# Performance work log

Hardware: AMD Instinct MI355X
Metric: run time of the kernel (lower is better)

The kernel has to match this reference:

```python
import jax, jax.numpy as jnp
import numpy as np

B, N, D = 4, 4096, 1024
QK = D // 8          # qk_dim_div = 8 -> 128
E = 2 * D            # expand_factor = 2 -> 2048


def setup_inputs() -> dict:
    key = jax.random.key(0)
    k1, k2, k3 = jax.random.split(key, 3)
    x = jax.random.normal(k1, (B, N, D), dtype=jnp.float32)
    # xavier-uniform-like scale for the fused expand / project weights
    expand = jax.random.normal(k2, (D, 2 * QK + 2 * E), dtype=jnp.float32) * np.sqrt(2.0 / (D + 2 * QK + 2 * E)).astype(np.float32)
    project = jax.random.normal(k3, (E, D), dtype=jnp.float32) * np.sqrt(2.0 / (E + D)).astype(np.float32)
    position_bias_mult = jnp.float32(4.0)
    return {"x": x, "expand": expand, "project": project, "position_bias_mult": position_bias_mult}


def _layer_norm(x, eps=1e-5):
    mu = jnp.mean(x, axis=-1, keepdims=True)
    var = jnp.mean(jnp.square(x - mu), axis=-1, keepdims=True)
    return (x - mu) * jax.lax.rsqrt(var + eps)


def reference(x, expand, project, position_bias_mult):
    d = x.shape[-1]
    qk, e = d // 8, 2 * d
    n = x.shape[1]

    nx = _layer_norm(x)
    h = nx @ expand                                    # [B, N, 2*qk + 2*e]
    q = h[..., :qk]
    k = h[..., qk:2 * qk]
    linear = h[..., 2 * qk:2 * qk + e]
    pre_gelu = h[..., 2 * qk + e:]

    gated = linear * jax.nn.gelu(pre_gelu, approximate=False)  # torch F.gelu = exact erf
    local = gated[..., :e - d]                          # [B, N, e-d]
    v = gated[..., e - d:]                              # [B, N, d]

    # learned sigmoid position bias under causal mask
    pos = jnp.arange(n)
    base = (pos[None, :] - pos[:, None]).astype(x.dtype)  # j - i
    causal = pos[None, :] <= pos[:, None]
    mask = jnp.where(causal, jax.nn.sigmoid(base + position_bias_mult), -jnp.inf)

    logits = jnp.einsum('bnq,bmq->bnm', q, k) / np.sqrt(qk).astype(np.float32) + mask
    scores = jax.nn.softmax(logits, axis=-1)            # [B, N, N]
    attn = jnp.einsum('bnm,bmd->bnd', scores, v)         # [B, N, d]

    return x + jnp.concatenate([local, attn], axis=-1) @ project
```

## Files before the change

### kernel.cpp

```cpp
#include <hip/hip_runtime.h>
#include <type_traits>

typedef __bf16 bf16x8 __attribute__((ext_vector_type(8)));
typedef __bf16 bf16x4v __attribute__((ext_vector_type(4)));
typedef float f32x4 __attribute__((ext_vector_type(4)));
typedef unsigned short u16x8 __attribute__((ext_vector_type(8)));
typedef unsigned short u16x4 __attribute__((ext_vector_type(4)));

#define NSEQ 4096
#define DM 1024
#define NBATCH 4

__device__ __forceinline__ unsigned short f2bf(float f) {
  unsigned u = __float_as_uint(f);
  u += 0x7FFFu + ((u >> 16) & 1u);
  return (unsigned short)(u >> 16);
}
__device__ __forceinline__ float bf2f(unsigned short h) {
  return __uint_as_float(((unsigned)h) << 16);
}
__device__ __forceinline__ float gelu_fast(float x) {
  const float y = 1.5957691216057308f * (x + 0.044715f * x * x * x);
  return x / (1.0f + __expf(-y));
}

__device__ __forceinline__ void gload_lds16(const unsigned short* src,
                                            unsigned short* dst) {
  __builtin_amdgcn_global_load_lds(
      (const __attribute__((address_space(1))) unsigned int*)src,
      (__attribute__((address_space(3))) unsigned int*)dst, 16, 0, 0);
}

#define BAR() asm volatile("s_barrier" ::: "memory")
#define VMCNT8() asm volatile("s_waitcnt vmcnt(8)" ::: "memory")

__device__ __forceinline__ int perm_col(int n) {
  if (n < 256) return n;
  int c = n - 256;
  if (c < 2048) return 256 + ((c >> 5) << 6) + (c & 31);
  c -= 2048;
  return 256 + ((c >> 5) << 6) + 32 + (c & 31);
}

__global__ __launch_bounds__(256) void ln_kernel(const float* __restrict__ x,
                                                 unsigned short* __restrict__ nx) {
  const int row = blockIdx.x;
  const int tid = threadIdx.x;
  const float4 v = reinterpret_cast<const float4*>(x + (size_t)row * DM)[tid];
  float s = v.x + v.y + v.z + v.w;
  float q = v.x * v.x + v.y * v.y + v.z * v.z + v.w * v.w;
#pragma unroll
  for (int off = 32; off > 0; off >>= 1) {
    s += __shfl_down(s, off);
    q += __shfl_down(q, off);
  }
  __shared__ float ss[4], sq[4];
  if ((tid & 63) == 0) {
    ss[tid >> 6] = s;
    sq[tid >> 6] = q;
  }
  __syncthreads();
  const float ts = ss[0] + ss[1] + ss[2] + ss[3];
  const float tq = sq[0] + sq[1] + sq[2] + sq[3];
  const float mu = ts * (1.0f / DM);
  const float var = tq * (1.0f / DM) - mu * mu;
  const float rs = rsqrtf(var + 1e-5f);
  u16x4 o;
  o[0] = f2bf((v.x - mu) * rs);
  o[1] = f2bf((v.y - mu) * rs);
  o[2] = f2bf((v.z - mu) * rs);
  o[3] = f2bf((v.w - mu) * rs);
  *reinterpret_cast<u16x4*>(nx + (size_t)row * DM + tid * 4) = o;
}

template <bool PERM>
__global__ __launch_bounds__(256) void tconv_kernel(const float* __restrict__ in,
                                                    unsigned short* __restrict__ out,
                                                    int K, int N) {
  __shared__ unsigned short tile[64][72];
  const int n0 = blockIdx.x * 64;
  const int k0 = blockIdx.y * 64;
  const int tid = threadIdx.x;
  const int lr = tid >> 4, lc = (tid & 15) * 4;
#pragma unroll
  for (int p = 0; p < 4; p++) {
    const int r = lr + p * 16;
    float4 v = *reinterpret_cast<const float4*>(in + (size_t)(k0 + r) * N + n0 + lc);
    tile[r][lc + 0] = f2bf(v.x);
    tile[r][lc + 1] = f2bf(v.y);
    tile[r][lc + 2] = f2bf(v.z);
    tile[r][lc + 3] = f2bf(v.w);
  }
  __syncthreads();
  const int nn = tid >> 2, kkg = (tid & 3) * 16;
  u16x8 o0, o1;
#pragma unroll
  for (int j = 0; j < 8; j++) {
    o0[j] = tile[kkg + j][nn];
    o1[j] = tile[kkg + 8 + j][nn];
  }
  const int orow = PERM ? perm_col(n0 + nn) : (n0 + nn);
  unsigned short* dst = out + (size_t)orow * K + k0 + kkg;
  *reinterpret_cast<u16x8*>(dst) = o0;
  *reinterpret_cast<u16x8*>(dst + 8) = o1;
}

template <int MODE>
__global__ __launch_bounds__(512, 2) void gemm256_kernel(
    const unsigned short* __restrict__ A, int lda,
    const unsigned short* __restrict__ Bt, int ldb, void* __restrict__ Cv,
    void* __restrict__ Cv2, int ldc, int K, int ntn,
    const float* __restrict__ X) {
  __shared__ unsigned short Ah[2][2][8192];
  __shared__ unsigned short Bh[2][2][8192];
  const int tid = threadIdx.x;
  const int lane = tid & 63;
  const int w = tid >> 6;
  const int lq = lane & 15;
  const int lg = lane >> 4;
  const int wm = w >> 2;
  const int wn = w & 3;
  const int bid = blockIdx.x;
  const int m0 = (bid / ntn) * 256;
  const int n0 = (bid % ntn) * 256;
  const int nk = K >> 6;

  const int g0 = w * 64 + lane;
  const int rowS = g0 >> 2;
  const int kcS = ((g0 & 3) * 8) ^ (((rowS >> 1) & 3) << 3);
  const unsigned short* Asrc = A + (size_t)(m0 + rowS) * lda + kcS;
  const unsigned short* Bsrc = Bt + (size_t)(n0 + rowS) * ldb + kcS;
  const size_t ldaj = (size_t)128 * lda;
  const size_t ldbj = (size_t)128 * ldb;
  const int dstW = w * 64 * 8;

  auto stageA = [&](int db, int kh, int kt2) {
    if (kt2 < nk) {
      const unsigned short* s = Asrc + (size_t)kt2 * 64 + kh * 32;
      unsigned short* d = &Ah[db][kh][0] + dstW;
      gload_lds16(s, d);
      gload_lds16(s + ldaj, d + 4096);
    }
  };
  auto stageB = [&](int db, int kh, int kt2) {
    if (kt2 < nk) {
      const unsigned short* s = Bsrc + (size_t)kt2 * 64 + kh * 32;
      unsigned short* d = &Bh[db][kh][0] + dstW;
      gload_lds16(s, d);
      gload_lds16(s + ldbj, d + 4096);
    }
  };

  f32x4 acc[8][4];
#pragma unroll
  for (int i = 0; i < 8; i++)
#pragma unroll
    for (int j = 0; j < 4; j++)
#pragma unroll
      for (int r = 0; r < 4; r++) acc[i][j][r] = 0.0f;

  stageA(0, 0, 0);
  stageB(0, 0, 0);
  stageA(0, 1, 0);
  stageB(0, 1, 0);
  stageA(1, 0, 1);
  stageB(1, 0, 1);
  VMCNT8();
  BAR();

  const int aBase = wm * 128;
  const int bBase = wn * 64;
  const int cSwz = (lg * 8) ^ (((lq >> 1) & 3) << 3);

#pragma unroll 1
  for (int kt = 0; kt < nk; ++kt) {
    const int buf = kt & 1;
    bf16x8 af[4], bf0[4], bf1[4];

#pragma unroll
    for (int i = 0; i < 4; i++)
      af[i] = *reinterpret_cast<const bf16x8*>(
          &Ah[buf][0][(aBase + i * 16 + lq) * 32 + cSwz]);
#pragma unroll
    for (int j = 0; j < 4; j++)
      bf0[j] = *reinterpret_cast<const bf16x8*>(
          &Bh[buf][0][(bBase + j * 16 + lq) * 32 + cSwz]);
    stageA(buf ^ 1, 1, kt + 1);
    BAR();
    __builtin_amdgcn_s_setprio(1);
#pragma unroll
    for (int i = 0; i < 4; i++)
#pragma unroll
      for (int j = 0; j < 4; j++)
        acc[i][j] =
            __builtin_amdgcn_mfma_f32_16x16x32_bf16(af[i], bf0[j], acc[i][j], 0, 0, 0);
    __builtin_amdgcn_s_setprio(0);
    BAR();

#pragma unroll
    for (int i = 0; i < 4; i++)
      af[i] = *reinterpret_cast<const bf16x8*>(
          &Ah[buf][0][(aBase + 64 + i * 16 + lq) * 32 + cSwz]);
    stageB(buf ^ 1, 1, kt + 1);
    VMCNT8();
    BAR();
    __builtin_amdgcn_s_setprio(1);
#pragma unroll
    for (int i = 0; i < 4; i++)
#pragma unroll
      for (int j = 0; j < 4; j++)
        acc[4 + i][j] = __builtin_amdgcn_mfma_f32_16x16x32_bf16(af[i], bf0[j],
                                                                acc[4 + i][j], 0, 0, 0);
    __builtin_amdgcn_s_setprio(0);
    BAR();

#pragma unroll
    for (int i = 0; i < 4; i++)
      af[i] = *reinterpret_cast<const bf16x8*>(
          &Ah[buf][1][(aBase + i * 16 + lq) * 32 + cSwz]);
#pragma unroll
    for (int j = 0; j < 4; j++)
      bf1[j] = *reinterpret_cast<const bf16x8*>(
          &Bh[buf][1][(bBase + j * 16 + lq) * 32 + cSwz]);
    stageA(buf, 0, kt + 2);
    BAR();
    __builtin_amdgcn_s_setprio(1);
#pragma unroll
    for (int i = 0; i < 4; i++)
#pragma unroll
      for (int j = 0; j < 4; j++)
        acc[i][j] =
            __builtin_amdgcn_mfma_f32_16x16x32_bf16(af[i], bf1[j], acc[i][j], 0, 0, 0);
    __builtin_amdgcn_s_setprio(0);
    BAR();

#pragma unroll
    for (int i = 0; i < 4; i++)
      af[i] = *reinterpret_cast<const bf16x8*>(
          &Ah[buf][1][(aBase + 64 + i * 16 + lq) * 32 + cSwz]);
    stageB(buf, 0, kt + 2);
    VMCNT8();
    BAR();
    __builtin_amdgcn_s_setprio(1);
#pragma unroll
    for (int i = 0; i < 4; i++)
#pragma unroll
      for (int j = 0; j < 4; j++)
        acc[4 + i][j] = __builtin_amdgcn_mfma_f32_16x16x32_bf16(af[i], bf1[j],
                                                                acc[4 + i][j], 0, 0, 0);
    __builtin_amdgcn_s_setprio(0);
    BAR();
  }

  if (MODE == 1) {
    float* C = reinterpret_cast<float*>(Cv);
#pragma unroll
    for (int I = 0; I < 8; I++)
#pragma unroll
      for (int j = 0; j < 4; j++)
#pragma unroll
        for (int r = 0; r < 4; r++) {
          const int row = m0 + wm * 128 + I * 16 + lg * 4 + r;
          const int col = n0 + wn * 64 + j * 16 + lq;
          const size_t off = (size_t)row * ldc + col;
          C[off] = X[off] + acc[I][j][r];
        }
  } else {
    unsigned short* concat = reinterpret_cast<unsigned short*>(Cv);
    unsigned short* vbuf = reinterpret_cast<unsigned short*>(Cv2);
    const int pi = (n0 + wn * 64) >> 6;
    const int cBase = pi * 32;
#pragma unroll
    for (int I = 0; I < 8; I++)
#pragma unroll
      for (int j = 0; j < 2; j++) {
        const int c = cBase + j * 16 + lq;
#pragma unroll
        for (int r = 0; r < 4; r++) {
          const int row = m0 + wm * 128 + I * 16 + lg * 4 + r;
          const float g = acc[I][j][r] * gelu_fast(acc[I][j + 2][r]);
          if (c < 1024)
            concat[(size_t)row * 2048 + c] = f2bf(g);
          else
            vbuf[(size_t)row * 1024 + (c - 1024)] = f2bf(g);
        }
      }
  }
}

__global__ __launch_bounds__(256, 4) void qk_kernel(
    const unsigned short* __restrict__ nx, const unsigned short* __restrict__ eT,
    unsigned short* __restrict__ qk) {
  __shared__ unsigned short As[128][64];
  __shared__ unsigned short Bs[128][64];
  const int tid = threadIdx.x;
  const int m0 = (blockIdx.x >> 1) * 128;
  const int n0 = (blockIdx.x & 1) * 128;
  const int lane = tid & 63;
  const int w = tid >> 6;
  const int lr = lane & 15;
  const int lg = lane >> 4;
  const int wr = (w >> 1) * 64;
  const int wc = (w & 1) * 64;
  const int rSwz = (lr & 7) << 3;

  f32x4 acc[4][4];
#pragma unroll
  for (int i = 0; i < 4; i++)
#pragma unroll
    for (int j = 0; j < 4; j++)
#pragma unroll
      for (int r = 0; r < 4; r++) acc[i][j][r] = 0.0f;

  for (int k0 = 0; k0 < 1024; k0 += 64) {
#pragma unroll
    for (int j = 0; j < 4; j++) {
      const int boff = w * 4096 + j * 1024 + lane * 16;
      const int row = boff >> 7;
      const int col = (((boff & 127) >> 1)) ^ ((row & 7) << 3);
      gload_lds16(nx + (size_t)(m0 + row) * DM + k0 + col,
                  &As[0][0] + (boff - lane * 16) / 2);
    }
#pragma unroll
    for (int j = 0; j < 4; j++) {
      const int boff = w * 4096 + j * 1024 + lane * 16;
      const int row = boff >> 7;
      const int col = (((boff & 127) >> 1)) ^ ((row & 7) << 3);
      gload_lds16(eT + (size_t)(n0 + row) * DM + k0 + col,
                  &Bs[0][0] + (boff - lane * 16) / 2);
    }
    __syncthreads();
#pragma unroll
    for (int kk = 0; kk < 64; kk += 32) {
      bf16x8 af[4], bfr[4];
#pragma unroll
      for (int i = 0; i < 4; i++)
        af[i] = *reinterpret_cast<const bf16x8*>(
            &As[wr + i * 16 + lr][(kk + lg * 8) ^ rSwz]);
#pragma unroll
      for (int j = 0; j < 4; j++)
        bfr[j] = *reinterpret_cast<const bf16x8*>(
            &Bs[wc + j * 16 + lr][(kk + lg * 8) ^ rSwz]);
#pragma unroll
      for (int i = 0; i < 4; i++)
#pragma unroll
        for (int j = 0; j < 4; j++)
          acc[i][j] = __builtin_amdgcn_mfma_f32_16x16x32_bf16(af[i], bfr[j],
                                                              acc[i][j], 0, 0, 0);
    }
    __syncthreads();
  }

#pragma unroll
  for (int i = 0; i < 4; i++)
#pragma unroll
    for (int j = 0; j < 4; j++)
#pragma unroll
      for (int r = 0; r < 4; r++) {
        const int row = m0 + wr + i * 16 + lg * 4 + r;
        const int col = n0 + wc + j * 16 + lr;
        qk[(size_t)row * 256 + col] = f2bf(acc[i][j][r]);
      }
}

__global__ __launch_bounds__(256) void vt_kernel(
    const unsigned short* __restrict__ vbuf, unsigned short* __restrict__ vT) {
  __shared__ unsigned short tbuf[64][72];
  const int n0 = blockIdx.x * 64;
  const int d0 = blockIdx.y * 64;
  const int b = blockIdx.z;
  const int tid = threadIdx.x;
#pragma unroll
  for (int p = 0; p < 2; p++) {
    const int r = p * 32 + (tid >> 3);
    const int cg = tid & 7;
    u16x8 v = *reinterpret_cast<const u16x8*>(
        vbuf + (size_t)(b * NSEQ + n0 + r) * 1024 + d0 + cg * 8);
    *reinterpret_cast<u16x8*>(&tbuf[r][cg * 8]) = v;
  }
  __syncthreads();
#pragma unroll
  for (int p = 0; p < 2; p++) {
    const int d = p * 32 + (tid >> 3);
    const int ng = tid & 7;
    u16x8 o;
#pragma unroll
    for (int j = 0; j < 8; j++) o[j] = tbuf[ng * 8 + j][d];
    *reinterpret_cast<u16x8*>(vT + (size_t)(b * DM + d0 + d) * NSEQ + n0 +
                              ng * 8) = o;
  }
}

#define P_TILE 16384
#define P_PER_B 8650752
__global__ __launch_bounds__(512, 4) void pk_kernel(
    const unsigned short* __restrict__ qk, const float* __restrict__ pbm_ptr,
    unsigned short* __restrict__ P, float* __restrict__ l) {
  __shared__ unsigned short Ks[128][136];
  const int tid = threadIdx.x;
  const int lane = tid & 63;
  const int w = tid >> 6;
  const int lq = lane & 15;
  const int lg = lane >> 4;
  const int bid = blockIdx.x;
  const int b = bid / 528;
  const int t = bid - b * 528;
  int qt = (int)((sqrtf((float)(8 * t + 1)) - 1.0f) * 0.5f);
  while ((qt + 1) * (qt + 2) / 2 <= t) ++qt;
  while (qt * (qt + 1) / 2 > t) --qt;
  const int kt = t - qt * (qt + 1) / 2;
  const float pbm = *pbm_ptr;
  const float SCALE = 0.08838834764831845f;

  const unsigned short* qb = qk + (size_t)b * NSEQ * 256;

#pragma unroll
  for (int p = 0; p < 4; p++) {
    const int task = tid + p * 512;
    const int row = task >> 4;
    const int ch = task & 15;
    bf16x8 v = *reinterpret_cast<const bf16x8*>(
        qb + (size_t)(kt * 128 + row) * 256 + 128 + ch * 8);
    *reinterpret_cast<bf16x8*>(&Ks[row][ch * 8]) = v;
  }
  const int qloc = w * 16 + lq;
  bf16x8 qf[4];
#pragma unroll
  for (int ks = 0; ks < 4; ks++)
    qf[ks] = *reinterpret_cast<const bf16x8*>(
        qb + (size_t)(qt * 128 + qloc) * 256 + ks * 32 + lg * 8);
  __syncthreads();

  f32x4 sa[8];
#pragma unroll
  for (int sub = 0; sub < 8; sub++)
#pragma unroll
    for (int r = 0; r < 4; r++) sa[sub][r] = 0.0f;
#pragma unroll
  for (int ks = 0; ks < 4; ks++)
#pragma unroll
    for (int sub = 0; sub < 8; sub++) {
      bf16x8 kf =
          *reinterpret_cast<const bf16x8*>(&Ks[sub * 16 + lq][ks * 32 + lg * 8]);
      sa[sub] = __builtin_amdgcn_mfma_f32_16x16x32_bf16(kf, qf[ks], sa[sub], 0, 0, 0);
    }
  const size_t KL = (size_t)(qt + 1) * 128;
  unsigned short* Prow = P + (size_t)b * P_PER_B +
                         (size_t)(qt * (qt + 1) / 2) * P_TILE + (size_t)qloc * KL +
                         kt * 128;
  float ps = 0.0f;
  const bool diag = (kt == qt);
#pragma unroll
  for (int sub = 0; sub < 8; sub++) {
    bf16x4v pv;
#pragma unroll
    for (int r = 0; r < 4; r++) {
      const int kvloc = sub * 16 + lg * 4 + r;
      float p;
      if (diag && kvloc > qloc) {
        p = 0.0f;
      } else {
        const float dn = (float)((kt - qt) * 128 + kvloc - qloc) + pbm;
        const float s = sa[sub][r] * SCALE + 1.0f / (1.0f + __expf(-dn));
        p = __expf(s);
      }
      ps += p;
      pv[r] = (__bf16)p;
    }
    *reinterpret_cast<bf16x4v*>(Prow + sub * 16 + lg * 4) = pv;
  }
  ps += __shfl_xor(ps, 16);
  ps += __shfl_xor(ps, 32);
  if (lane < 16) atomicAdd(&l[b * NSEQ + qt * 128 + w * 16 + lane], ps);
}

__global__ __launch_bounds__(256, 4) void pv_kernel(
    const unsigned short* __restrict__ P, const unsigned short* __restrict__ vT,
    const float* __restrict__ l, unsigned short* __restrict__ concat) {
  __shared__ unsigned short As[128][64];
  __shared__ unsigned short Bs[128][64];
  const int tid = threadIdx.x;
  const int bid = blockIdx.x;
  const int qt = 31 - (bid >> 5);
  const int rest = bid & 31;
  const int b = rest >> 3;
  const int nt = rest & 7;
  const int KL = (qt + 1) * 128;
  const unsigned short* A =
      P + (size_t)b * P_PER_B + (size_t)(qt * (qt + 1) / 2) * P_TILE;
  const unsigned short* Bt = vT + (size_t)b * DM * NSEQ;
  const int n0 = nt * 128;
  const int lane = tid & 63;
  const int w = tid >> 6;
  const int lr = lane & 15;
  const int lg = lane >> 4;
  const int wr = (w >> 1) * 64;
  const int wc = (w & 1) * 64;
  const int rSwz = (lr & 7) << 3;

  f32x4 acc[4][4];
#pragma unroll
  for (int i = 0; i < 4; i++)
#pragma unroll
    for (int j = 0; j < 4; j++)
#pragma unroll
      for (int r = 0; r < 4; r++) acc[i][j][r] = 0.0f;

  for (int k0 = 0; k0 < KL; k0 += 64) {
#pragma unroll
    for (int j = 0; j < 4; j++) {
      const int boff = w * 4096 + j * 1024 + lane * 16;
      const int row = boff >> 7;
      const int col = (((boff & 127) >> 1)) ^ ((row & 7) << 3);
      gload_lds16(A + (size_t)row * KL + k0 + col,
                  &As[0][0] + (boff - lane * 16) / 2);
    }
#pragma unroll
    for (int j = 0; j < 4; j++) {
      const int boff = w * 4096 + j * 1024 + lane * 16;
      const int row = boff >> 7;
      const int col = (((boff & 127) >> 1)) ^ ((row & 7) << 3);
      gload_lds16(Bt + (size_t)(n0 + row) * NSEQ + k0 + col,
                  &Bs[0][0] + (boff - lane * 16) / 2);
    }
    __syncthreads();
#pragma unroll
    for (int kk = 0; kk < 64; kk += 32) {
      bf16x8 af[4], bfr[4];
#pragma unroll
      for (int i = 0; i < 4; i++)
        af[i] = *reinterpret_cast<const bf16x8*>(
            &As[wr + i * 16 + lr][(kk + lg * 8) ^ rSwz]);
#pragma unroll
      for (int j = 0; j < 4; j++)
        bfr[j] = *reinterpret_cast<const bf16x8*>(
            &Bs[wc + j * 16 + lr][(kk + lg * 8) ^ rSwz]);
#pragma unroll
      for (int i = 0; i < 4; i++)
#pragma unroll
        for (int j = 0; j < 4; j++)
          acc[i][j] = __builtin_amdgcn_mfma_f32_16x16x32_bf16(af[i], bfr[j],
                                                              acc[i][j], 0, 0, 0);
    }
    __syncthreads();
  }

  const float* lb = l + b * NSEQ + qt * 128;
#pragma unroll
  for (int i = 0; i < 4; i++) {
    f32x4 lv = *reinterpret_cast<const f32x4*>(&lb[wr + i * 16 + lg * 4]);
    f32x4 inv;
#pragma unroll
    for (int r = 0; r < 4; r++) inv[r] = 1.0f / lv[r];
#pragma unroll
    for (int j = 0; j < 4; j++)
#pragma unroll
      for (int r = 0; r < 4; r++) {
        const int grow = b * NSEQ + qt * 128 + wr + i * 16 + lg * 4 + r;
        const int col = 1024 + n0 + wc + j * 16 + lr;
        concat[(size_t)grow * 2048 + col] = f2bf(acc[i][j][r] * inv[r]);
      }
  }
}

extern "C" void kernel_launch(void* const* d_in, const int* in_sizes, int n_in,
                              void* d_out, int out_size, void* d_ws,
                              size_t ws_size, hipStream_t stream) {
  (void)in_sizes;
  (void)n_in;
  (void)out_size;
  const float* x = (const float*)d_in[0];
  const float* expand = (const float*)d_in[1];
  const float* project = (const float*)d_in[2];
  const float* pbm = (const float*)d_in[3];
  float* out = (float*)d_out;

  const size_t QK_BYTES = (size_t)16384 * 256 * 2;
  const size_t VBUF_BYTES = (size_t)16384 * 1024 * 2;
  const size_t P_BYTES = (size_t)NBATCH * P_PER_B * 2;
  const size_t L_BYTES = (size_t)NBATCH * NSEQ * 4;
  const size_t GH_BYTES = (size_t)16384 * 4096 * 2;
  const size_t CAT_BYTES = (size_t)16384 * 2048 * 2;
  const size_t NX_BYTES = (size_t)16384 * DM * 2;
  if (ws_size < QK_BYTES + GH_BYTES + CAT_BYTES + NX_BYTES) return;

  char* ws = (char*)d_ws;
  unsigned short* qk = (unsigned short*)ws;
  unsigned short* vbuf = (unsigned short*)(ws + QK_BYTES);
  unsigned short* P = (unsigned short*)(ws + QK_BYTES + VBUF_BYTES);
  float* l = (float*)(ws + QK_BYTES + VBUF_BYTES + P_BYTES);
  unsigned short* expandT =
      (unsigned short*)(ws + QK_BYTES + VBUF_BYTES + P_BYTES + L_BYTES);
  unsigned short* concat = (unsigned short*)(ws + QK_BYTES + GH_BYTES);
  unsigned short* nx = (unsigned short*)(ws + QK_BYTES + GH_BYTES + CAT_BYTES);
  unsigned short* vT = nx;
  unsigned short* projectT = nx;

  tconv_kernel<true><<<dim3(68, 16), 256, 0, stream>>>(expand, expandT, 1024, 4352);
  ln_kernel<<<16384, 256, 0, stream>>>(x, nx);
  qk_kernel<<<dim3(256), 256, 0, stream>>>(nx, expandT, qk);
  gemm256_kernel<2><<<dim3(64 * 16), 512, 0, stream>>>(
      nx, DM, expandT + (size_t)256 * DM, DM, (void*)concat, (void*)vbuf, 0, DM,
      16, nullptr);
  vt_kernel<<<dim3(64, 16, 4), 256, 0, stream>>>(vbuf, vT);
  hipMemsetAsync(l, 0, L_BYTES, stream);
  pk_kernel<<<dim3(NBATCH * 528), 512, 0, stream>>>(qk, pbm, P, l);
  pv_kernel<<<dim3(1024), 256, 0, stream>>>(P, vT, l, concat);
  tconv_kernel<false><<<dim3(16, 32), 256, 0, stream>>>(project, projectT, 2048, DM);
  gemm256_kernel<1><<<dim3(64 * 4), 512, 0, stream>>>(
      concat, 2048, projectT, 2048, (void*)out, nullptr, DM, 2048, 4, x);
}
```

Measured before the change: 453.2 us.

## Fuse V transpose into expand GEMM epilogue and stage output stores through LDS

The expand GEMM epilogue now stages its gated bf16 tile in shared memory. The local half is written to concat as coalesced 16-byte row stores, and the V half is written already transposed into vT, so the separate vt_kernel and its vbuf round-trip go away. The pv_kernel epilogue likewise stages its output in LDS and writes coalesced 16-byte chunks instead of scattered 2-byte stores. LDS arrays are unified into flat buffers so they can be reused for the epilogue, at the cost of an extra vmcnt(0) wait and barriers at the end.

```diff
diff --git a/kernel.cpp b/kernel.cpp
--- a/kernel.cpp
+++ b/kernel.cpp
@@ -33,6 +33,7 @@
 
 #define BAR() asm volatile("s_barrier" ::: "memory")
 #define VMCNT8() asm volatile("s_waitcnt vmcnt(8)" ::: "memory")
+#define VMCNT0() asm volatile("s_waitcnt vmcnt(0)" ::: "memory")
 
 __device__ __forceinline__ int perm_col(int n) {
   if (n < 256) return n;
@@ -111,8 +112,7 @@
     const unsigned short* __restrict__ Bt, int ldb, void* __restrict__ Cv,
     void* __restrict__ Cv2, int ldc, int K, int ntn,
     const float* __restrict__ X) {
-  __shared__ unsigned short Ah[2][2][8192];
-  __shared__ unsigned short Bh[2][2][8192];
+  __shared__ unsigned short G[65536];
   const int tid = threadIdx.x;
   const int lane = tid & 63;
   const int w = tid >> 6;
@@ -125,6 +125,9 @@
   const int n0 = (bid % ntn) * 256;
   const int nk = K >> 6;
 
+  auto AH = [&](int db, int kh) { return G + (db * 2 + kh) * 8192; };
+  auto BH = [&](int db, int kh) { return G + 32768 + (db * 2 + kh) * 8192; };
+
   const int g0 = w * 64 + lane;
   const int rowS = g0 >> 2;
   const int kcS = ((g0 & 3) * 8) ^ (((rowS >> 1) & 3) << 3);
@@ -137,7 +140,7 @@
   auto stageA = [&](int db, int kh, int kt2) {
     if (kt2 < nk) {
       const unsigned short* s = Asrc + (size_t)kt2 * 64 + kh * 32;
-      unsigned short* d = &Ah[db][kh][0] + dstW;
+      unsigned short* d = AH(db, kh) + dstW;
       gload_lds16(s, d);
       gload_lds16(s + ldaj, d + 4096);
     }
@@ -145,7 +148,7 @@
   auto stageB = [&](int db, int kh, int kt2) {
     if (kt2 < nk) {
       const unsigned short* s = Bsrc + (size_t)kt2 * 64 + kh * 32;
-      unsigned short* d = &Bh[db][kh][0] + dstW;
+      unsigned short* d = BH(db, kh) + dstW;
       gload_lds16(s, d);
       gload_lds16(s + ldbj, d + 4096);
     }
@@ -180,11 +183,11 @@
 #pragma unroll
     for (int i = 0; i < 4; i++)
       af[i] = *reinterpret_cast<const bf16x8*>(
-          &Ah[buf][0][(aBase + i * 16 + lq) * 32 + cSwz]);
+          AH(buf, 0) + (aBase + i * 16 + lq) * 32 + cSwz);
 #pragma unroll
     for (int j = 0; j < 4; j++)
       bf0[j] = *reinterpret_cast<const bf16x8*>(
-          &Bh[buf][0][(bBase + j * 16 + lq) * 32 + cSwz]);
+          BH(buf, 0) + (bBase + j * 16 + lq) * 32 + cSwz);
     stageA(buf ^ 1, 1, kt + 1);
     BAR();
     __builtin_amdgcn_s_setprio(1);
@@ -200,7 +203,7 @@
 #pragma unroll
     for (int i = 0; i < 4; i++)
       af[i] = *reinterpret_cast<const bf16x8*>(
-          &Ah[buf][0][(aBase + 64 + i * 16 + lq) * 32 + cSwz]);
+          AH(buf, 0) + (aBase + 64 + i * 16 + lq) * 32 + cSwz);
     stageB(buf ^ 1, 1, kt + 1);
     VMCNT8();
     BAR();
@@ -217,11 +220,11 @@
 #pragma unroll
     for (int i = 0; i < 4; i++)
       af[i] = *reinterpret_cast<const bf16x8*>(
-          &Ah[buf][1][(aBase + i * 16 + lq) * 32 + cSwz]);
+          AH(buf, 1) + (aBase + i * 16 + lq) * 32 + cSwz);
 #pragma unroll
     for (int j = 0; j < 4; j++)
       bf1[j] = *reinterpret_cast<const bf16x8*>(
-          &Bh[buf][1][(bBase + j * 16 + lq) * 32 + cSwz]);
+          BH(buf, 1) + (bBase + j * 16 + lq) * 32 + cSwz);
     stageA(buf, 0, kt + 2);
     BAR();
     __builtin_amdgcn_s_setprio(1);
@@ -237,7 +240,7 @@
 #pragma unroll
     for (int i = 0; i < 4; i++)
       af[i] = *reinterpret_cast<const bf16x8*>(
-          &Ah[buf][1][(aBase + 64 + i * 16 + lq) * 32 + cSwz]);
+          AH(buf, 1) + (aBase + 64 + i * 16 + lq) * 32 + cSwz);
     stageB(buf, 0, kt + 2);
     VMCNT8();
     BAR();
@@ -266,25 +269,55 @@
           C[off] = X[off] + acc[I][j][r];
         }
   } else {
+    VMCNT0();
+    BAR();
     unsigned short* concat = reinterpret_cast<unsigned short*>(Cv);
-    unsigned short* vbuf = reinterpret_cast<unsigned short*>(Cv2);
-    const int pi = (n0 + wn * 64) >> 6;
-    const int cBase = pi * 32;
-#pragma unroll
-    for (int I = 0; I < 8; I++)
-#pragma unroll
-      for (int j = 0; j < 2; j++) {
-        const int c = cBase + j * 16 + lq;
-#pragma unroll
-        for (int r = 0; r < 4; r++) {
-          const int row = m0 + wm * 128 + I * 16 + lg * 4 + r;
-          const float g = acc[I][j][r] * gelu_fast(acc[I][j + 2][r]);
-          if (c < 1024)
-            concat[(size_t)row * 2048 + c] = f2bf(g);
-          else
-            vbuf[(size_t)row * 1024 + (c - 1024)] = f2bf(g);
-        }
+    unsigned short* vT = reinterpret_cast<unsigned short*>(Cv2);
+    if (n0 < 2048) {
+      const int c0 = n0 >> 1;
+#pragma unroll
+      for (int I = 0; I < 8; I++)
+#pragma unroll
+        for (int j = 0; j < 2; j++)
+#pragma unroll
+          for (int r = 0; r < 4; r++) {
+            const float g = acc[I][j][r] * gelu_fast(acc[I][j + 2][r]);
+            G[(wm * 128 + I * 16 + lg * 4 + r) * 136 + wn * 32 + j * 16 + lq] =
+                f2bf(g);
+          }
+      BAR();
+#pragma unroll
+      for (int it = 0; it < 8; ++it) {
+        const int chunk = tid + it * 512;
+        const int row = chunk >> 4, cc = chunk & 15;
+        *reinterpret_cast<u16x8*>(concat + (size_t)(m0 + row) * 2048 + c0 +
+                                  cc * 8) =
+            *reinterpret_cast<const u16x8*>(&G[row * 136 + cc * 8]);
       }
+    } else {
+      const int d0 = (n0 >> 1) - 1024;
+      const int b = m0 >> 12;
+      const int nn0 = m0 & 4095;
+#pragma unroll
+      for (int I = 0; I < 8; I++)
+#pragma unroll
+        for (int j = 0; j < 2; j++)
+#pragma unroll
+          for (int r = 0; r < 4; r++) {
+            const float g = acc[I][j][r] * gelu_fast(acc[I][j + 2][r]);
+            G[(wn * 32 + j * 16 + lq) * 264 + wm * 128 + I * 16 + lg * 4 + r] =
+                f2bf(g);
+          }
+      BAR();
+#pragma unroll
+      for (int it = 0; it < 8; ++it) {
+        const int chunk = tid + it * 512;
+        const int d = chunk >> 5, cc = chunk & 31;
+        *reinterpret_cast<u16x8*>(vT + (size_t)(b * 1024 + d0 + d) * 4096 +
+                                  nn0 + cc * 8) =
+            *reinterpret_cast<const u16x8*>(&G[d * 264 + cc * 8]);
+      }
+    }
   }
 }
 
@@ -361,34 +394,6 @@
         const int col = n0 + wc + j * 16 + lr;
         qk[(size_t)row * 256 + col] = f2bf(acc[i][j][r]);
       }
-}
-
-__global__ __launch_bounds__(256) void vt_kernel(
-    const unsigned short* __restrict__ vbuf, unsigned short* __restrict__ vT) {
-  __shared__ unsigned short tbuf[64][72];
-  const int n0 = blockIdx.x * 64;
-  const int d0 = blockIdx.y * 64;
-  const int b = blockIdx.z;
-  const int tid = threadIdx.x;
-#pragma unroll
-  for (int p = 0; p < 2; p++) {
-    const int r = p * 32 + (tid >> 3);
-    const int cg = tid & 7;
-    u16x8 v = *reinterpret_cast<const u16x8*>(
-        vbuf + (size_t)(b * NSEQ + n0 + r) * 1024 + d0 + cg * 8);
-    *reinterpret_cast<u16x8*>(&tbuf[r][cg * 8]) = v;
-  }
-  __syncthreads();
-#pragma unroll
-  for (int p = 0; p < 2; p++) {
-    const int d = p * 32 + (tid >> 3);
-    const int ng = tid & 7;
-    u16x8 o;
-#pragma unroll
-    for (int j = 0; j < 8; j++) o[j] = tbuf[ng * 8 + j][d];
-    *reinterpret_cast<u16x8*>(vT + (size_t)(b * DM + d0 + d) * NSEQ + n0 +
-                              ng * 8) = o;
-  }
 }
 
 #define P_TILE 16384
@@ -477,8 +482,9 @@
 __global__ __launch_bounds__(256, 4) void pv_kernel(
     const unsigned short* __restrict__ P, const unsigned short* __restrict__ vT,
     const float* __restrict__ l, unsigned short* __restrict__ concat) {
-  __shared__ unsigned short As[128][64];
-  __shared__ unsigned short Bs[128][64];
+  __shared__ unsigned short LDSp[17408];
+  unsigned short* Asb = LDSp;
+  unsigned short* Bsb = LDSp + 8192;
   const int tid = threadIdx.x;
   const int bid = blockIdx.x;
   const int qt = 31 - (bid >> 5);
@@ -513,7 +519,7 @@
       const int row = boff >> 7;
       const int col = (((boff & 127) >> 1)) ^ ((row & 7) << 3);
       gload_lds16(A + (size_t)row * KL + k0 + col,
-                  &As[0][0] + (boff - lane * 16) / 2);
+                  Asb + (boff - lane * 16) / 2);
     }
 #pragma unroll
     for (int j = 0; j < 4; j++) {
@@ -521,7 +527,7 @@
       const int row = boff >> 7;
       const int col = (((boff & 127) >> 1)) ^ ((row & 7) << 3);
       gload_lds16(Bt + (size_t)(n0 + row) * NSEQ + k0 + col,
-                  &Bs[0][0] + (boff - lane * 16) / 2);
+                  Bsb + (boff - lane * 16) / 2);
     }
     __syncthreads();
 #pragma unroll
@@ -530,11 +536,11 @@
 #pragma unroll
       for (int i = 0; i < 4; i++)
         af[i] = *reinterpret_cast<const bf16x8*>(
-            &As[wr + i * 16 + lr][(kk + lg * 8) ^ rSwz]);
+            Asb + (wr + i * 16 + lr) * 64 + ((kk + lg * 8) ^ rSwz));
 #pragma unroll
       for (int j = 0; j < 4; j++)
         bfr[j] = *reinterpret_cast<const bf16x8*>(
-            &Bs[wc + j * 16 + lr][(kk + lg * 8) ^ rSwz]);
+            Bsb + (wc + j * 16 + lr) * 64 + ((kk + lg * 8) ^ rSwz));
 #pragma unroll
       for (int i = 0; i < 4; i++)
 #pragma unroll
@@ -555,11 +561,19 @@
 #pragma unroll
     for (int j = 0; j < 4; j++)
 #pragma unroll
-      for (int r = 0; r < 4; r++) {
-        const int grow = b * NSEQ + qt * 128 + wr + i * 16 + lg * 4 + r;
-        const int col = 1024 + n0 + wc + j * 16 + lr;
-        concat[(size_t)grow * 2048 + col] = f2bf(acc[i][j][r] * inv[r]);
-      }
+      for (int r = 0; r < 4; r++)
+        LDSp[(wr + i * 16 + lg * 4 + r) * 136 + wc + j * 16 + lr] =
+            f2bf(acc[i][j][r] * inv[r]);
+  }
+  __syncthreads();
+#pragma unroll
+  for (int it = 0; it < 8; ++it) {
+    const int chunk = tid + it * 256;
+    const int row = chunk >> 4, cc = chunk & 15;
+    *reinterpret_cast<u16x8*>(concat +
+                              (size_t)(b * NSEQ + qt * 128 + row) * 2048 + 1024 +
+                              n0 + cc * 8) =
+        *reinterpret_cast<const u16x8*>(&LDSp[row * 136 + cc * 8]);
   }
 }
 
@@ -576,7 +590,7 @@
   float* out = (float*)d_out;
 
   const size_t QK_BYTES = (size_t)16384 * 256 * 2;
-  const size_t VBUF_BYTES = (size_t)16384 * 1024 * 2;
+  const size_t VT_BYTES = (size_t)16384 * 1024 * 2;
   const size_t P_BYTES = (size_t)NBATCH * P_PER_B * 2;
   const size_t L_BYTES = (size_t)NBATCH * NSEQ * 4;
   const size_t GH_BYTES = (size_t)16384 * 4096 * 2;
@@ -586,23 +600,21 @@
 
   char* ws = (char*)d_ws;
   unsigned short* qk = (unsigned short*)ws;
-  unsigned short* vbuf = (unsigned short*)(ws + QK_BYTES);
-  unsigned short* P = (unsigned short*)(ws + QK_BYTES + VBUF_BYTES);
-  float* l = (float*)(ws + QK_BYTES + VBUF_BYTES + P_BYTES);
+  unsigned short* vT = (unsigned short*)(ws + QK_BYTES);
+  unsigned short* P = (unsigned short*)(ws + QK_BYTES + VT_BYTES);
+  float* l = (float*)(ws + QK_BYTES + VT_BYTES + P_BYTES);
   unsigned short* expandT =
-      (unsigned short*)(ws + QK_BYTES + VBUF_BYTES + P_BYTES + L_BYTES);
+      (unsigned short*)(ws + QK_BYTES + VT_BYTES + P_BYTES + L_BYTES);
   unsigned short* concat = (unsigned short*)(ws + QK_BYTES + GH_BYTES);
   unsigned short* nx = (unsigned short*)(ws + QK_BYTES + GH_BYTES + CAT_BYTES);
-  unsigned short* vT = nx;
   unsigned short* projectT = nx;
 
   tconv_kernel<true><<<dim3(68, 16), 256, 0, stream>>>(expand, expandT, 1024, 4352);
   ln_kernel<<<16384, 256, 0, stream>>>(x, nx);
   qk_kernel<<<dim3(256), 256, 0, stream>>>(nx, expandT, qk);
   gemm256_kernel<2><<<dim3(64 * 16), 512, 0, stream>>>(
-      nx, DM, expandT + (size_t)256 * DM, DM, (void*)concat, (void*)vbuf, 0, DM,
+      nx, DM, expandT + (size_t)256 * DM, DM, (void*)concat, (void*)vT, 0, DM,
       16, nullptr);
-  vt_kernel<<<dim3(64, 16, 4), 256, 0, stream>>>(vbuf, vT);
   hipMemsetAsync(l, 0, L_BYTES, stream);
   pk_kernel<<<dim3(NBATCH * 528), 512, 0, stream>>>(qk, pbm, P, l);
   pv_kernel<<<dim3(1024), 256, 0, stream>>>(P, vT, l, concat);
```

After: 428.6 us. -5.4%, faster.
